# Kernel tuning notes

Hardware: AMD Instinct MI355X
Metric: run time of the kernel (lower is better)

The kernel has to match this reference:

```python
import jax, jax.numpy as jnp
import numpy as np

B, H, S, DH = 2, 16, 2048, 64

def setup_inputs() -> dict:
    key = jax.random.key(0)
    k1, k2, k3 = jax.random.split(key, 3)
    return {
        "query": jax.random.normal(k1, (B, H, S, DH), dtype=jnp.float32),
        "key": jax.random.normal(k2, (B, H, S, DH), dtype=jnp.float32),
        "value": jax.random.normal(k3, (B, H, S, DH), dtype=jnp.float32),
        "key_padding_mask": jnp.zeros((B, S), dtype=bool),
    }

def reference(query, key, value, key_padding_mask):
    # scores: [B, H, Sq, Sk]
    scale = 1.0 / jnp.sqrt(jnp.asarray(query.shape[-1], query.dtype))
    scores = jnp.einsum("bhqd,bhkd->bhqk", query, key) * scale
    # key padding mask broadcasts over heads and query positions
    scores = jnp.where(key_padding_mask[:, None, None, :], -jnp.inf, scores)
    attn = jax.nn.softmax(scores, axis=-1)
    # dropout is identity in eval mode (deterministic reference)
    out = jnp.einsum("bhqk,bhkd->bhqd", attn, value)
    # [B, H, S, Dh] -> [B, S, H*Dh]
    b, h, s, dh = out.shape
    return out.transpose(0, 2, 1, 3).reshape(b, s, h * dh)
```

## Files before the change

### kernel.cpp

```cpp
#include <hip/hip_runtime.h>

typedef __attribute__((ext_vector_type(4))) float f32x4;
typedef __attribute__((ext_vector_type(4))) short s16x4;
typedef __attribute__((ext_vector_type(8))) short s16x8;

constexpr int Bn = 2, Hn = 16, Sn = 2048, DHn = 64;
constexpr int TQ = 64;
constexpr int TK = 64;
constexpr int NT = Sn / TK;
constexpr int TILE_SH = TK * DHn;
constexpr float SHIFT = 16.0f;

__device__ __forceinline__ unsigned pk2(float a, float b) {
  unsigned ua = __builtin_bit_cast(unsigned, a);
  unsigned ub = __builtin_bit_cast(unsigned, b);
  ua += 0x7fffu + ((ua >> 16) & 1u);
  ub += 0x7fffu + ((ub >> 16) & 1u);
  return (ua >> 16) | (ub & 0xffff0000u);
}

__device__ __forceinline__ unsigned pkP(float a, float b) {
#if __has_builtin(__builtin_amdgcn_cvt_pk_bf16_f32)
  auto r = __builtin_amdgcn_cvt_pk_bf16_f32(a, b);
  unsigned u;
  __builtin_memcpy(&u, &r, 4);
  return u;
#else
  return pk2(a, b);
#endif
}

__device__ __forceinline__ float fexp2(float x) {
#if __has_builtin(__builtin_amdgcn_exp2f)
  return __builtin_amdgcn_exp2f(x);
#else
  return exp2f(x);
#endif
}

__global__ __launch_bounds__(256, 4)
void prepack_kernel(const float* __restrict__ Kg, const float* __restrict__ Vg,
                    const unsigned char* __restrict__ maskg,
                    short* __restrict__ Kp, short* __restrict__ Vp,
                    float* __restrict__ biasg) {
  const int blk = blockIdx.x;
  const int tid = threadIdx.x;
  const float* Kt = Kg + (size_t)blk * TILE_SH;
  const float* Vt = Vg + (size_t)blk * TILE_SH;
  short* Kd = Kp + (size_t)blk * TILE_SH;
  short* Vd = Vp + (size_t)blk * TILE_SH;

  {
    const int r = tid >> 2;
    const int cb = (tid & 3) * 2;
#pragma unroll
    for (int cc = 0; cc < 2; ++cc) {
      int c = cb + cc;
      const float4* p = (const float4*)(Kt + (size_t)r * DHn + c * 8);
      float4 x = p[0], y = p[1];
      union { unsigned u[4]; s16x8 v; } tmp;
      tmp.u[0] = pk2(x.x, x.y); tmp.u[1] = pk2(x.z, x.w);
      tmp.u[2] = pk2(y.x, y.y); tmp.u[3] = pk2(y.z, y.w);
      *(s16x8*)&Kd[r * 64 + (c ^ (r & 7)) * 8] = tmp.v;
    }
  }
  {
    const int d = tid & 63;
    const int kb = (tid >> 6) * 16;
#pragma unroll
    for (int cc = 0; cc < 2; ++cc) {
      int k0 = kb + cc * 8;
      float v0[8];
#pragma unroll
      for (int j = 0; j < 8; ++j) v0[j] = Vt[(size_t)(k0 + j) * DHn + d];
      union { unsigned u[4]; s16x8 v; } tmp;
      tmp.u[0] = pk2(v0[0], v0[1]); tmp.u[1] = pk2(v0[2], v0[3]);
      tmp.u[2] = pk2(v0[4], v0[5]); tmp.u[3] = pk2(v0[6], v0[7]);
      int c = k0 >> 3;
      *(s16x8*)&Vd[d * 64 + (c ^ (d & 7)) * 8] = tmp.v;
    }
  }
  if (tid < TK) {
    const int bh = blk >> 5, t = blk & 31, b = bh >> 4;
    biasg[b * Sn + t * TK + tid] = maskg[b * Sn + t * TK + tid] ? -1e30f : -SHIFT;
  }
}

__global__ __launch_bounds__(128, 2)
void fattn_kernel(const float* __restrict__ Qg, const short* __restrict__ Kp,
                  const short* __restrict__ Vp, const float* __restrict__ biasg,
                  float* __restrict__ Og) {
  __shared__ __align__(16) short Psh[2 * 32 * 64];

  const int tid  = threadIdx.x;
  const int w    = tid >> 6;
  const int lane = tid & 63;
  const int n    = lane & 15;
  const int q4   = lane >> 4;
  const int swz  = n & 7;

  const int blk = blockIdx.x;
  const int bh  = blk & 31;
  const int qt  = blk >> 5;
  const int b   = bh >> 4;
  const int h   = bh & 15;

  const float* Qb  = Qg + (size_t)bh * Sn * DHn;
  const short* Kt0 = Kp + (size_t)bh * NT * TILE_SH;
  const short* Vt0 = Vp + (size_t)bh * NT * TILE_SH;
  const float* bq0 = biasg + (size_t)b * Sn;

  const int q0 = qt * TQ + w * 32;

  const float c1 = 0.125f * 1.4426950408889634f;
  s16x8 qf[2][2];
#pragma unroll
  for (int qg = 0; qg < 2; ++qg) {
    const float* qrow = Qb + (size_t)(q0 + qg * 16 + n) * DHn;
#pragma unroll
    for (int kc = 0; kc < 2; ++kc) {
      const float4* p = (const float4*)(qrow + kc * 32 + q4 * 8);
      float4 x = p[0], y = p[1];
      union { unsigned u[4]; s16x8 v; } tmp;
      tmp.u[0] = pk2(x.x * c1, x.y * c1);
      tmp.u[1] = pk2(x.z * c1, x.w * c1);
      tmp.u[2] = pk2(y.x * c1, y.y * c1);
      tmp.u[3] = pk2(y.z * c1, y.w * c1);
      qf[qg][kc] = tmp.v;
    }
  }

  const int c0    = q4 ^ swz;
  const int offA  = n * 64 + c0 * 8;
  const int offB  = n * 64 + (c0 ^ 4) * 8;
  const int prowA = (w * 32 + n) * 64;
  const int pc    = (q4 >> 1) ^ swz;
  const int pwo   = (q4 & 1) * 4;

  s16x8 ones;
#pragma unroll
  for (int i = 0; i < 8; ++i) ones[i] = (short)0x3F80;

  f32x4 Oa[2][4];
#pragma unroll
  for (int qg = 0; qg < 2; ++qg)
#pragma unroll
    for (int na = 0; na < 4; ++na) Oa[qg][na] = (f32x4){0.f, 0.f, 0.f, 0.f};
  f32x4 lacc[2] = {(f32x4){0.f, 0.f, 0.f, 0.f}, (f32x4){0.f, 0.f, 0.f, 0.f}};

  auto load_tile = [&](s16x8 kf[4][2], s16x8 vf[4][2], int t) {
    const short* Ka = Kt0 + (size_t)t * TILE_SH;
    const short* Va = Vt0 + (size_t)t * TILE_SH;
#pragma unroll
    for (int mc = 0; mc < 4; ++mc) {
      kf[mc][0] = *(const s16x8*)&Ka[mc * 1024 + offA];
      kf[mc][1] = *(const s16x8*)&Ka[mc * 1024 + offB];
      vf[mc][0] = *(const s16x8*)&Va[mc * 1024 + offA];
      vf[mc][1] = *(const s16x8*)&Va[mc * 1024 + offB];
    }
  };

  auto compute_tile = [&](s16x8 kf[4][2], s16x8 vf[4][2], int t) {
    f32x4 bias[4];
    {
      const float* bq = bq0 + t * TK + q4 * 4;
#pragma unroll
      for (int mc = 0; mc < 4; ++mc) bias[mc] = *(const f32x4*)(bq + mc * 16);
    }
#pragma unroll
    for (int qg = 0; qg < 2; ++qg) {
      f32x4 sa[4];
#pragma unroll
      for (int mc = 0; mc < 4; ++mc) sa[mc] = bias[mc];
#pragma unroll
      for (int mc = 0; mc < 4; ++mc)
#pragma unroll
        for (int kc = 0; kc < 2; ++kc)
          sa[mc] = __builtin_amdgcn_mfma_f32_16x16x32_bf16(kf[mc][kc], qf[qg][kc], sa[mc], 0, 0, 0);

      const int prow = prowA + qg * (16 * 64);
#pragma unroll
      for (int mc = 0; mc < 4; ++mc) {
        float p0 = fexp2(sa[mc][0]);
        float p1 = fexp2(sa[mc][1]);
        float p2 = fexp2(sa[mc][2]);
        float p3 = fexp2(sa[mc][3]);
        union { unsigned u[2]; s16x4 v4; } pw;
        pw.u[0] = pkP(p0, p1);
        pw.u[1] = pkP(p2, p3);
        *(s16x4*)&Psh[prow + ((pc ^ (2 * mc)) * 8) + pwo] = pw.v4;
      }
    }
#pragma unroll
    for (int qg = 0; qg < 2; ++qg) {
      const int prow = prowA + qg * (16 * 64);
      s16x8 pf[2];
      pf[0] = *(const s16x8*)&Psh[prow + ((q4 ^ swz) * 8)];
      pf[1] = *(const s16x8*)&Psh[prow + (((4 + q4) ^ swz) * 8)];
      lacc[qg] = __builtin_amdgcn_mfma_f32_16x16x32_bf16(pf[0], ones, lacc[qg], 0, 0, 0);
      lacc[qg] = __builtin_amdgcn_mfma_f32_16x16x32_bf16(pf[1], ones, lacc[qg], 0, 0, 0);
#pragma unroll
      for (int na = 0; na < 4; ++na)
#pragma unroll
        for (int kc = 0; kc < 2; ++kc)
          Oa[qg][na] = __builtin_amdgcn_mfma_f32_16x16x32_bf16(pf[kc], vf[na][kc], Oa[qg][na], 0, 0, 0);
    }
  };

  s16x8 kfA[4][2], vfA[4][2], kfB[4][2], vfB[4][2];
  load_tile(kfA, vfA, 0);
  for (int t = 0; t < NT; t += 2) {
    if (t + 1 < NT) load_tile(kfB, vfB, t + 1);
    compute_tile(kfA, vfA, t);
    if (t + 2 < NT) load_tile(kfA, vfA, t + 2);
    if (t + 1 < NT) compute_tile(kfB, vfB, t + 1);
  }

#pragma unroll
  for (int qg = 0; qg < 2; ++qg) {
#pragma unroll
    for (int r = 0; r < 4; ++r) {
      float inv = 1.0f / lacc[qg][r];
      int q = q0 + qg * 16 + q4 * 4 + r;
      float* orow = Og + (size_t)(b * Sn + q) * (Hn * DHn) + h * DHn;
#pragma unroll
      for (int na = 0; na < 4; ++na)
        orow[na * 16 + n] = Oa[qg][na][r] * inv;
    }
  }
}

extern "C" void kernel_launch(void* const* d_in, const int* in_sizes, int n_in,
                              void* d_out, int out_size, void* d_ws, size_t ws_size,
                              hipStream_t stream) {
  (void)in_sizes; (void)n_in; (void)ws_size; (void)out_size;
  const float* Q = (const float*)d_in[0];
  const float* K = (const float*)d_in[1];
  const float* V = (const float*)d_in[2];
  const unsigned char* mask = (const unsigned char*)d_in[3];
  float* out = (float*)d_out;

  short* Kp = (short*)d_ws;
  short* Vp = Kp + (size_t)Bn * Hn * Sn * DHn;
  float* biasg = (float*)(Vp + (size_t)Bn * Hn * Sn * DHn);

  hipLaunchKernelGGL(prepack_kernel, dim3(Bn * Hn * NT), dim3(256), 0, stream,
                     K, V, mask, Kp, Vp, biasg);
  hipLaunchKernelGGL(fattn_kernel, dim3(Bn * Hn * (Sn / TQ)), dim3(128), 0, stream,
                     Q, Kp, Vp, biasg, out);
}
```

Measured before the change: 167.0 us.

## Split key range across two wave pairs and merge partial outputs in LDS

```diff
diff --git a/kernel.cpp b/kernel.cpp
--- a/kernel.cpp
+++ b/kernel.cpp
@@ -65,19 +65,25 @@
     }
   }
   {
-    const int d = tid & 63;
-    const int kb = (tid >> 6) * 16;
-#pragma unroll
-    for (int cc = 0; cc < 2; ++cc) {
-      int k0 = kb + cc * 8;
-      float v0[8];
-#pragma unroll
-      for (int j = 0; j < 8; ++j) v0[j] = Vt[(size_t)(k0 + j) * DHn + d];
-      union { unsigned u[4]; s16x8 v; } tmp;
-      tmp.u[0] = pk2(v0[0], v0[1]); tmp.u[1] = pk2(v0[2], v0[3]);
-      tmp.u[2] = pk2(v0[4], v0[5]); tmp.u[3] = pk2(v0[6], v0[7]);
-      int c = k0 >> 3;
-      *(s16x8*)&Vd[d * 64 + (c ^ (d & 7)) * 8] = tmp.v;
+    const int tx = tid & 15, ty = tid >> 4;
+    const int d0 = tx * 4, k0 = ty * 4;
+    float4 r_[4];
+#pragma unroll
+    for (int i = 0; i < 4; ++i)
+      r_[i] = *(const float4*)(Vt + (size_t)(k0 + i) * DHn + d0);
+    float c_[4][4] = {
+        {r_[0].x, r_[1].x, r_[2].x, r_[3].x},
+        {r_[0].y, r_[1].y, r_[2].y, r_[3].y},
+        {r_[0].z, r_[1].z, r_[2].z, r_[3].z},
+        {r_[0].w, r_[1].w, r_[2].w, r_[3].w}};
+    const int c = k0 >> 3;
+#pragma unroll
+    for (int j = 0; j < 4; ++j) {
+      int d = d0 + j;
+      union { unsigned u[2]; s16x4 v4; } st;
+      st.u[0] = pk2(c_[j][0], c_[j][1]);
+      st.u[1] = pk2(c_[j][2], c_[j][3]);
+      *(s16x4*)&Vd[d * 64 + ((c ^ (d & 7)) * 8) + (k0 & 7)] = st.v4;
     }
   }
   if (tid < TK) {
@@ -86,11 +92,12 @@
   }
 }
 
-__global__ __launch_bounds__(128, 2)
+__global__ __launch_bounds__(256, 4)
 void fattn_kernel(const float* __restrict__ Qg, const short* __restrict__ Kp,
                   const short* __restrict__ Vp, const float* __restrict__ biasg,
                   float* __restrict__ Og) {
-  __shared__ __align__(16) short Psh[2 * 32 * 64];
+  __shared__ __align__(16) short Psh[4 * 32 * 64];
+  __shared__ __align__(16) float Xch[2 * 64 * 41];
 
   const int tid  = threadIdx.x;
   const int w    = tid >> 6;
@@ -98,6 +105,8 @@
   const int n    = lane & 15;
   const int q4   = lane >> 4;
   const int swz  = n & 7;
+  const int kh   = w >> 1;
+  const int wq   = w & 1;
 
   const int blk = blockIdx.x;
   const int bh  = blk & 31;
@@ -110,7 +119,7 @@
   const short* Vt0 = Vp + (size_t)bh * NT * TILE_SH;
   const float* bq0 = biasg + (size_t)b * Sn;
 
-  const int q0 = qt * TQ + w * 32;
+  const int q0 = qt * TQ + wq * 32;
 
   const float c1 = 0.125f * 1.4426950408889634f;
   s16x8 qf[2][2];
@@ -207,25 +216,45 @@
     }
   };
 
+  const int t0 = kh * 16;
   s16x8 kfA[4][2], vfA[4][2], kfB[4][2], vfB[4][2];
-  load_tile(kfA, vfA, 0);
-  for (int t = 0; t < NT; t += 2) {
-    if (t + 1 < NT) load_tile(kfB, vfB, t + 1);
-    compute_tile(kfA, vfA, t);
-    if (t + 2 < NT) load_tile(kfA, vfA, t + 2);
-    if (t + 1 < NT) compute_tile(kfB, vfB, t + 1);
-  }
-
-#pragma unroll
-  for (int qg = 0; qg < 2; ++qg) {
-#pragma unroll
-    for (int r = 0; r < 4; ++r) {
-      float inv = 1.0f / lacc[qg][r];
-      int q = q0 + qg * 16 + q4 * 4 + r;
-      float* orow = Og + (size_t)(b * Sn + q) * (Hn * DHn) + h * DHn;
+  load_tile(kfA, vfA, t0);
+  for (int tt = 0; tt < 16; tt += 2) {
+    load_tile(kfB, vfB, t0 + tt + 1);
+    compute_tile(kfA, vfA, t0 + tt);
+    if (tt + 2 < 16) load_tile(kfA, vfA, t0 + tt + 2);
+    compute_tile(kfB, vfB, t0 + tt + 1);
+  }
+
+  __syncthreads();
+  const int xbase = (wq * 64 + lane) * 41;
+  if (kh == 1) {
+#pragma unroll
+    for (int qg = 0; qg < 2; ++qg) {
 #pragma unroll
       for (int na = 0; na < 4; ++na)
-        orow[na * 16 + n] = Oa[qg][na][r] * inv;
+#pragma unroll
+        for (int r = 0; r < 4; ++r)
+          Xch[xbase + qg * 16 + na * 4 + r] = Oa[qg][na][r];
+#pragma unroll
+      for (int r = 0; r < 4; ++r)
+        Xch[xbase + 32 + qg * 4 + r] = lacc[qg][r];
+    }
+  }
+  __syncthreads();
+  if (kh == 0) {
+#pragma unroll
+    for (int qg = 0; qg < 2; ++qg) {
+#pragma unroll
+      for (int r = 0; r < 4; ++r) {
+        float l = lacc[qg][r] + Xch[xbase + 32 + qg * 4 + r];
+        float inv = 1.0f / l;
+        int q = q0 + qg * 16 + q4 * 4 + r;
+        float* orow = Og + (size_t)(b * Sn + q) * (Hn * DHn) + h * DHn;
+#pragma unroll
+        for (int na = 0; na < 4; ++na)
+          orow[na * 16 + n] = (Oa[qg][na][r] + Xch[xbase + qg * 16 + na * 4 + r]) * inv;
+      }
     }
   }
 }
@@ -246,6 +275,6 @@
 
   hipLaunchKernelGGL(prepack_kernel, dim3(Bn * Hn * NT), dim3(256), 0, stream,
                      K, V, mask, Kp, Vp, biasg);
-  hipLaunchKernelGGL(fattn_kernel, dim3(Bn * Hn * (Sn / TQ)), dim3(128), 0, stream,
+  hipLaunchKernelGGL(fattn_kernel, dim3(Bn * Hn * (Sn / TQ)), dim3(256), 0, stream,
                      Q, Kp, Vp, biasg, out);
 }
```

After: 348.3 us. +108.6%, slower.
